# Optimization experiments

Measured on AMD Instinct MI355X. Metric: run time of the kernel, lower is better.

Reference implementation:

```python
import jax, jax.numpy as jnp
import numpy as np

N, D, E, H = 16384, 1024, 4, 4096
TEMP = 1.0

def setup_inputs() -> dict:
    key = jax.random.key(0)
    ks = jax.random.split(key, 6)
    s_in = 1.0 / np.sqrt(D)
    s_h = 1.0 / np.sqrt(H)
    s_g = 1.0 / np.sqrt(2 * D)
    return {
        "q": jax.random.normal(ks[0], (N, D), jnp.float32),
        "k": jax.random.normal(ks[1], (N, D), jnp.float32),
        "W1": jax.random.normal(ks[2], (E, D, H), jnp.float32) * s_in,
        "b1": jnp.zeros((E, H), jnp.float32),
        "W2": jax.random.normal(ks[3], (E, H, D), jnp.float32) * s_h,
        "b2": jnp.zeros((E, D), jnp.float32),
        "Wg": jax.random.normal(ks[4], (2 * D, 4), jnp.float32) * s_g,
        "bg": jnp.zeros((4,), jnp.float32),
    }

def reference(q, k, W1, b1, W2, b2, Wg, bg):
    # Run all E experts on the same tokens via batched GEMMs.
    h = jax.nn.relu(jnp.einsum('nd,edh->neh', q, W1) + b1)        # [N,E,H]
    q_pred = jnp.einsum('neh,ehd->ned', h, W2) + b2               # [N,E,D]
    # Gate: Linear(dim*2 -> 4) on concat(q,k), softmax over experts.
    logits = (jnp.concatenate([q, k], axis=-1) @ Wg + bg) / TEMP  # [N,4]
    gate = jax.nn.softmax(logits, axis=-1)                        # [N,E]
    return jnp.einsum('ned,ne->nd', q_pred, gate)                 # [N,D]
```

## Files before the change

kernel.cpp:

```cpp
#include <hip/hip_runtime.h>
#include <hip/hip_bf16.h>

#define N_TOK 16384
#define DIM   1024
#define NEXP  4
#define HID   4096

typedef __attribute__((ext_vector_type(8))) short short8;
typedef __attribute__((ext_vector_type(4))) short short4v;
typedef __attribute__((ext_vector_type(4))) float float4v;

static __device__ __forceinline__ short f2bf(float f) {
  __hip_bfloat16 h = __float2bfloat16(f);
  return *reinterpret_cast<short*>(&h);
}

#define GLOAD_LDS16(gsrc, ldst)                                                            \
  __builtin_amdgcn_global_load_lds((const __attribute__((address_space(1))) void*)(gsrc),  \
                                   (__attribute__((address_space(3))) void*)(ldst), 16, 0, 0)

__global__ void gate_kernel(const float* __restrict__ q, const float* __restrict__ k,
                            const float* __restrict__ Wg, const float* __restrict__ bg,
                            float* __restrict__ gate) {
  const int wave = threadIdx.x >> 6, lane = threadIdx.x & 63;
  const int n = blockIdx.x * 4 + wave;
  const float* qr = q + (size_t)n * DIM;
  const float* kr = k + (size_t)n * DIM;
  float s0 = 0.f, s1 = 0.f, s2 = 0.f, s3 = 0.f;
  for (int i = 0; i < DIM / 64; ++i) {
    int d = i * 64 + lane;
    float x = qr[d];
    float4 w = *(const float4*)(Wg + (size_t)d * 4);
    s0 += x * w.x; s1 += x * w.y; s2 += x * w.z; s3 += x * w.w;
    float y = kr[d];
    float4 w2 = *(const float4*)(Wg + (size_t)(DIM + d) * 4);
    s0 += y * w2.x; s1 += y * w2.y; s2 += y * w2.z; s3 += y * w2.w;
  }
  for (int off = 32; off; off >>= 1) {
    s0 += __shfl_xor(s0, off);
    s1 += __shfl_xor(s1, off);
    s2 += __shfl_xor(s2, off);
    s3 += __shfl_xor(s3, off);
  }
  if (lane == 0) {
    float l0 = s0 + bg[0], l1 = s1 + bg[1], l2 = s2 + bg[2], l3 = s3 + bg[3];
    float m = fmaxf(fmaxf(l0, l1), fmaxf(l2, l3));
    float e0 = expf(l0 - m), e1 = expf(l1 - m), e2 = expf(l2 - m), e3 = expf(l3 - m);
    float inv = 1.f / (e0 + e1 + e2 + e3);
    float4 g; g.x = e0 * inv; g.y = e1 * inv; g.z = e2 * inv; g.w = e3 * inv;
    *(float4*)(gate + (size_t)n * 4) = g;
  }
}

__global__ void convert_bf16_kernel(const float* __restrict__ in, short* __restrict__ out, int n4) {
  int stride = gridDim.x * blockDim.x;
  for (int i = blockIdx.x * blockDim.x + threadIdx.x; i < n4; i += stride) {
    float4 v = *(const float4*)(in + (size_t)i * 4);
    short4v o;
    o[0] = f2bf(v.x); o[1] = f2bf(v.y); o[2] = f2bf(v.z); o[3] = f2bf(v.w);
    *(short4v*)(out + (size_t)i * 4) = o;
  }
}

__global__ void transpose_bf16_kernel(const float* __restrict__ in, short* __restrict__ out,
                                      int R, int C) {
  __shared__ float tile[64][65];
  const size_t eoff = (size_t)blockIdx.z * (size_t)R * C;
  const float* src = in + eoff;
  short* dst = out + eoff;
  const int r0 = blockIdx.y * 64, c0 = blockIdx.x * 64;
  const int tc = threadIdx.x & 63, tr = threadIdx.x >> 6;
#pragma unroll
  for (int p = 0; p < 16; ++p) {
    int r = p * 4 + tr;
    tile[r][tc] = src[(size_t)(r0 + r) * C + (c0 + tc)];
  }
  __syncthreads();
#pragma unroll
  for (int p = 0; p < 16; ++p) {
    int i = p * 4 + tr;
    dst[(size_t)(c0 + i) * R + (r0 + tc)] = f2bf(tile[tc][i]);
  }
}

template <int MODE>
__global__ __launch_bounds__(256, 2)
void gemm_kernel(const short* __restrict__ A, const short* __restrict__ Bt, int K,
                 const float* __restrict__ bias, const float* __restrict__ gate4,
                 short* __restrict__ HsOut, float* __restrict__ FOut, int ldc, int accumulate) {
  __shared__ short sA[128 * 64];
  __shared__ short sB[128 * 64];
  const int t = threadIdx.x;
  const int m0 = blockIdx.y * 128;
  const int n0 = blockIdx.x * 128;
  const int lane = t & 63;
  const int wave = t >> 6;
  const int wm = (wave >> 1) * 64;
  const int wn = (wave & 1) * 64;
  const int r16 = lane & 15;
  const int kg = lane >> 4;

  float4v acc[4][4];
#pragma unroll
  for (int m = 0; m < 4; ++m)
#pragma unroll
    for (int n = 0; n < 4; ++n) acc[m][n] = (float4v)0.0f;

  for (int k0 = 0; k0 < K; k0 += 64) {
#pragma unroll
    for (int i = 0; i < 4; ++i) {
      int c = i * 256 + t;
      int row = c >> 3;
      int jc = (c & 7) ^ (row & 7);
      GLOAD_LDS16(A + (size_t)(m0 + row) * K + k0 + jc * 8, &sA[c * 8]);
      GLOAD_LDS16(Bt + (size_t)(n0 + row) * K + k0 + jc * 8, &sB[c * 8]);
    }
    __syncthreads();
#pragma unroll
    for (int kk = 0; kk < 2; ++kk) {
      short8 af[4], bfr[4];
#pragma unroll
      for (int m = 0; m < 4; ++m) {
        int row = wm + m * 16 + r16;
        int jc = (kk * 4 + kg) ^ (row & 7);
        af[m] = *(const short8*)&sA[row * 64 + jc * 8];
      }
#pragma unroll
      for (int n = 0; n < 4; ++n) {
        int row = wn + n * 16 + r16;
        int jc = (kk * 4 + kg) ^ (row & 7);
        bfr[n] = *(const short8*)&sB[row * 64 + jc * 8];
      }
#pragma unroll
      for (int m = 0; m < 4; ++m)
#pragma unroll
        for (int n = 0; n < 4; ++n)
          acc[m][n] = __builtin_amdgcn_mfma_f32_16x16x32_bf16(af[m], bfr[n], acc[m][n], 0, 0, 0);
    }
    __syncthreads();
  }

#pragma unroll
  for (int m = 0; m < 4; ++m) {
    int rbase = m0 + wm + m * 16 + kg * 4;
#pragma unroll
    for (int n = 0; n < 4; ++n) {
      int col = n0 + wn + n * 16 + r16;
      float bcol = bias[col];
#pragma unroll
      for (int r = 0; r < 4; ++r) {
        int grow = rbase + r;
        float g = gate4[(size_t)grow * 4];
        float v = acc[m][n][r];
        if (MODE == 1) {
          v += bcol;
          v = fmaxf(v, 0.f);
          v *= g;
          HsOut[(size_t)grow * ldc + col] = f2bf(v);
        } else {
          v += g * bcol;
          size_t oi = (size_t)grow * ldc + col;
          if (accumulate) v += FOut[oi];
          FOut[oi] = v;
        }
      }
    }
  }
}

extern "C" void kernel_launch(void* const* d_in, const int* in_sizes, int n_in,
                              void* d_out, int out_size, void* d_ws, size_t ws_size,
                              hipStream_t stream) {
  const float* q  = (const float*)d_in[0];
  const float* k  = (const float*)d_in[1];
  const float* W1 = (const float*)d_in[2];
  const float* b1 = (const float*)d_in[3];
  const float* W2 = (const float*)d_in[4];
  const float* b2 = (const float*)d_in[5];
  const float* Wg = (const float*)d_in[6];
  const float* bg = (const float*)d_in[7];
  float* out = (float*)d_out;

  char* ws = (char*)d_ws;
  size_t off = 0;
  float* gate = (float*)(ws + off); off += (size_t)N_TOK * 4 * sizeof(float);
  short* qb   = (short*)(ws + off); off += (size_t)N_TOK * DIM * 2;
  short* W1t  = (short*)(ws + off); off += (size_t)NEXP * (size_t)DIM * HID * 2;
  short* W2t  = (short*)(ws + off); off += (size_t)NEXP * (size_t)HID * DIM * 2;
  short* Hs   = (short*)(ws + off);

  size_t avail = (ws_size > off) ? (ws_size - off) : 0;
  long long mc = (long long)(avail / ((size_t)HID * 2));
  mc &= ~127LL;
  if (mc < 128) mc = 128;
  if (mc > N_TOK) mc = N_TOK;
  const int max_chunk = (int)mc;

  gate_kernel<<<dim3(N_TOK / 4), dim3(256), 0, stream>>>(q, k, Wg, bg, gate);
  convert_bf16_kernel<<<dim3(2048), dim3(256), 0, stream>>>(q, qb, N_TOK * DIM / 4);
  transpose_bf16_kernel<<<dim3(HID / 64, DIM / 64, NEXP), dim3(256), 0, stream>>>(W1, W1t, DIM, HID);
  transpose_bf16_kernel<<<dim3(DIM / 64, HID / 64, NEXP), dim3(256), 0, stream>>>(W2, W2t, HID, DIM);

  for (int cb = 0; cb < N_TOK; cb += max_chunk) {
    int rows = (N_TOK - cb < max_chunk) ? (N_TOK - cb) : max_chunk;
    for (int e = 0; e < NEXP; ++e) {
      gemm_kernel<1><<<dim3(HID / 128, rows / 128), dim3(256), 0, stream>>>(
          qb + (size_t)cb * DIM, W1t + (size_t)e * HID * DIM, DIM,
          b1 + (size_t)e * HID, gate + (size_t)cb * 4 + e,
          Hs, (float*)nullptr, HID, 0);
      gemm_kernel<2><<<dim3(DIM / 128, rows / 128), dim3(256), 0, stream>>>(
          Hs, W2t + (size_t)e * DIM * HID, HID,
          b2 + (size_t)e * DIM, gate + (size_t)cb * 4 + e,
          (short*)nullptr, out + (size_t)cb * DIM, DIM, e > 0);
    }
  }
}
```

Before: 1.372 ms.

## Use 256x256 double-buffered GEMM and fuse experts into two concatenated GEMMs

```diff
diff --git a/kernel.cpp b/kernel.cpp
--- a/kernel.cpp
+++ b/kernel.cpp
@@ -63,11 +63,10 @@
 }
 
 __global__ void transpose_bf16_kernel(const float* __restrict__ in, short* __restrict__ out,
-                                      int R, int C) {
+                                      int R, int C, int ldo, int z_row, int z_col) {
   __shared__ float tile[64][65];
-  const size_t eoff = (size_t)blockIdx.z * (size_t)R * C;
-  const float* src = in + eoff;
-  short* dst = out + eoff;
+  const int z = blockIdx.z;
+  const float* src = in + (size_t)z * R * C;
   const int r0 = blockIdx.y * 64, c0 = blockIdx.x * 64;
   const int tc = threadIdx.x & 63, tr = threadIdx.x >> 6;
 #pragma unroll
@@ -79,89 +78,167 @@
 #pragma unroll
   for (int p = 0; p < 16; ++p) {
     int i = p * 4 + tr;
-    dst[(size_t)(c0 + i) * R + (r0 + tc)] = f2bf(tile[tc][i]);
-  }
+    out[(size_t)(z * z_row + c0 + i) * ldo + z * z_col + (r0 + tc)] = f2bf(tile[tc][i]);
+  }
+}
+
+template <int QM, bool READB, bool VMWAIT>
+__device__ __forceinline__ void do_phase(const short* pA, const short* pB,
+                                         short8 (&af)[4], short8 (&bf)[4],
+                                         float4v (&acc)[8][4]) {
+#pragma unroll
+  for (int m4 = 0; m4 < 4; ++m4)
+    af[m4] = *(const short8*)(pA + QM * 4096 + m4 * 1024);
+  if (READB) {
+#pragma unroll
+    for (int n4 = 0; n4 < 4; ++n4)
+      bf[n4] = *(const short8*)(pB + n4 * 1024);
+  }
+  __builtin_amdgcn_s_barrier();
+  asm volatile("s_waitcnt lgkmcnt(0)" ::: "memory");
+  __builtin_amdgcn_sched_barrier(0);
+  __builtin_amdgcn_s_setprio(1);
+#pragma unroll
+  for (int m4 = 0; m4 < 4; ++m4)
+#pragma unroll
+    for (int n4 = 0; n4 < 4; ++n4)
+      acc[QM * 4 + m4][n4] =
+          __builtin_amdgcn_mfma_f32_16x16x32_bf16(af[m4], bf[n4], acc[QM * 4 + m4][n4], 0, 0, 0);
+  __builtin_amdgcn_s_setprio(0);
+  if (VMWAIT) asm volatile("s_waitcnt vmcnt(0)" ::: "memory");
+  __builtin_amdgcn_sched_barrier(0);
+  __builtin_amdgcn_s_barrier();
 }
 
 template <int MODE>
-__global__ __launch_bounds__(256, 2)
-void gemm_kernel(const short* __restrict__ A, const short* __restrict__ Bt, int K,
-                 const float* __restrict__ bias, const float* __restrict__ gate4,
-                 short* __restrict__ HsOut, float* __restrict__ FOut, int ldc, int accumulate) {
-  __shared__ short sA[128 * 64];
-  __shared__ short sB[128 * 64];
-  const int t = threadIdx.x;
-  const int m0 = blockIdx.y * 128;
-  const int n0 = blockIdx.x * 128;
-  const int lane = t & 63;
-  const int wave = t >> 6;
-  const int wm = (wave >> 1) * 64;
-  const int wn = (wave & 1) * 64;
-  const int r16 = lane & 15;
-  const int kg = lane >> 4;
-
-  float4v acc[4][4];
-#pragma unroll
-  for (int m = 0; m < 4; ++m)
+__global__ __launch_bounds__(512, 2)
+void gemm256(const short* __restrict__ A, const short* __restrict__ Bt, int K, int ldb,
+             int NTN, const float* __restrict__ bias, const float* __restrict__ gate,
+             int ecol_off, int e0, int e1, int accum,
+             short* __restrict__ OutB, float* __restrict__ OutF, int ldc) {
+  __shared__ short sA[32768];
+  __shared__ short sB[32768];
+
+  const int nwg = gridDim.x;
+  const int NTM = nwg / NTN;
+  {
+  }
+  int bid = blockIdx.x;
+  int qd = nwg >> 3, rm = nwg & 7;
+  int xcd = bid & 7, idx = bid >> 3;
+  int swz = (xcd < rm ? xcd * (qd + 1) : rm * (qd + 1) + (xcd - rm) * qd) + idx;
+  const int tpg = 8 * NTN;
+  int g = swz / tpg;
+  int lg = swz % tpg;
+  int gm0 = g * 8;
+  int gsz = NTM - gm0; if (gsz > 8) gsz = 8;
+  const int tile_m = gm0 + lg % gsz;
+  const int tile_n = lg / gsz;
+  const int m0 = tile_m * 256;
+  const int n0 = tile_n * 256;
+
+  const int tid = threadIdx.x;
+  const int lane = tid & 63;
+  const int wid = tid >> 6;
+  const int wm = wid >> 2, wn = wid & 3;
+  const int r16 = lane & 15, kg = lane >> 4;
+  const int rowL = tid >> 3;
+  const int gc8 = (((tid & 7) ^ (rowL & 7)) * 8);
+  const int st8 = tid * 8;
+  const int sw0 = (kg ^ (r16 & 7)) * 8;
+  const int sw1 = ((4 + kg) ^ (r16 & 7)) * 8;
+  const int aoff0 = (wm * 128 + r16) * 64 + sw0;
+  const int aoff1 = (wm * 128 + r16) * 64 + sw1;
+  const int boff0 = (wn * 64 + r16) * 64 + sw0;
+  const int boff1 = (wn * 64 + r16) * 64 + sw1;
+
+  const short* aSrc = A + (size_t)(m0 + rowL) * K + gc8;
+  const short* bSrc = Bt + (size_t)(n0 + rowL) * ldb + gc8;
+
+  float4v acc[8][4];
+#pragma unroll
+  for (int m = 0; m < 8; ++m)
 #pragma unroll
     for (int n = 0; n < 4; ++n) acc[m][n] = (float4v)0.0f;
 
-  for (int k0 = 0; k0 < K; k0 += 64) {
-#pragma unroll
-    for (int i = 0; i < 4; ++i) {
-      int c = i * 256 + t;
-      int row = c >> 3;
-      int jc = (c & 7) ^ (row & 7);
-      GLOAD_LDS16(A + (size_t)(m0 + row) * K + k0 + jc * 8, &sA[c * 8]);
-      GLOAD_LDS16(Bt + (size_t)(n0 + row) * K + k0 + jc * 8, &sB[c * 8]);
-    }
-    __syncthreads();
-#pragma unroll
-    for (int kk = 0; kk < 2; ++kk) {
-      short8 af[4], bfr[4];
-#pragma unroll
-      for (int m = 0; m < 4; ++m) {
-        int row = wm + m * 16 + r16;
-        int jc = (kk * 4 + kg) ^ (row & 7);
-        af[m] = *(const short8*)&sA[row * 64 + jc * 8];
+#pragma unroll
+  for (int s = 0; s < 4; ++s) {
+    GLOAD_LDS16(aSrc + (size_t)s * 64 * K, sA + s * 4096 + st8);
+    GLOAD_LDS16(bSrc + (size_t)s * 64 * ldb, sB + s * 4096 + st8);
+  }
+  asm volatile("s_waitcnt vmcnt(0)" ::: "memory");
+  __builtin_amdgcn_s_barrier();
+
+  const int T = K >> 6;
+  const short* aN = aSrc + 64;
+  const short* bN = bSrc + 64;
+  int cur = 0;
+  short8 af[4], bf[4];
+  for (int t = 0; t < T; ++t) {
+    const int co = cur << 14;
+    const int po = (cur ^ 1) << 14;
+    const bool next = (t + 1 < T);
+    const short* pA0 = sA + co + aoff0;
+    const short* pA1 = sA + co + aoff1;
+    const short* pB0 = sB + co + boff0;
+    const short* pB1 = sB + co + boff1;
+    if (next) {
+#pragma unroll
+      for (int s = 0; s < 4; ++s) GLOAD_LDS16(aN + (size_t)s * 64 * K, sA + po + s * 4096 + st8);
+    }
+    do_phase<0, true, false>(pA0, pB0, af, bf, acc);
+    if (next) {
+#pragma unroll
+      for (int s = 0; s < 4; ++s) GLOAD_LDS16(bN + (size_t)s * 64 * ldb, sB + po + s * 4096 + st8);
+    }
+    do_phase<1, false, false>(pA0, pB0, af, bf, acc);
+    do_phase<0, true, false>(pA1, pB1, af, bf, acc);
+    do_phase<1, false, true>(pA1, pB1, af, bf, acc);
+    aN += 64;
+    bN += 64;
+    cur ^= 1;
+  }
+
+  const int rowb = m0 + wm * 128 + kg * 4;
+  const int colb = n0 + wn * 64 + r16;
+  if (MODE == 1) {
+    const int e = (ecol_off + n0) >> 12;
+#pragma unroll
+    for (int m4 = 0; m4 < 8; ++m4) {
+      int r0a = rowb + m4 * 16;
+#pragma unroll
+      for (int r = 0; r < 4; ++r) {
+        int row = r0a + r;
+        float g = gate[(size_t)row * 4 + e];
+#pragma unroll
+        for (int n4 = 0; n4 < 4; ++n4) {
+          int col = colb + n4 * 16;
+          float v = acc[m4][n4][r] + bias[ecol_off + col];
+          OutB[(size_t)row * ldc + col] = f2bf(fmaxf(v, 0.f) * g);
+        }
       }
-#pragma unroll
-      for (int n = 0; n < 4; ++n) {
-        int row = wn + n * 16 + r16;
-        int jc = (kk * 4 + kg) ^ (row & 7);
-        bfr[n] = *(const short8*)&sB[row * 64 + jc * 8];
-      }
-#pragma unroll
-      for (int m = 0; m < 4; ++m)
-#pragma unroll
-        for (int n = 0; n < 4; ++n)
-          acc[m][n] = __builtin_amdgcn_mfma_f32_16x16x32_bf16(af[m], bfr[n], acc[m][n], 0, 0, 0);
-    }
-    __syncthreads();
-  }
-
-#pragma unroll
-  for (int m = 0; m < 4; ++m) {
-    int rbase = m0 + wm + m * 16 + kg * 4;
-#pragma unroll
-    for (int n = 0; n < 4; ++n) {
-      int col = n0 + wn + n * 16 + r16;
-      float bcol = bias[col];
+    }
+  } else {
+#pragma unroll
+    for (int m4 = 0; m4 < 8; ++m4) {
+      int r0a = rowb + m4 * 16;
 #pragma unroll
       for (int r = 0; r < 4; ++r) {
-        int grow = rbase + r;
-        float g = gate4[(size_t)grow * 4];
-        float v = acc[m][n][r];
-        if (MODE == 1) {
-          v += bcol;
-          v = fmaxf(v, 0.f);
-          v *= g;
-          HsOut[(size_t)grow * ldc + col] = f2bf(v);
-        } else {
-          v += g * bcol;
-          size_t oi = (size_t)grow * ldc + col;
-          if (accumulate) v += FOut[oi];
-          FOut[oi] = v;
+        int row = r0a + r;
+        float4 gv = *(const float4*)(gate + (size_t)row * 4);
+#pragma unroll
+        for (int n4 = 0; n4 < 4; ++n4) {
+          int col = colb + n4 * 16;
+          float bt;
+          if (e0 == 0 && e1 == 4)
+            bt = gv.x * bias[col] + gv.y * bias[1024 + col] + gv.z * bias[2048 + col] +
+                 gv.w * bias[3072 + col];
+          else
+            bt = gate[(size_t)row * 4 + e0] * bias[e0 * 1024 + col];
+          float v = acc[m4][n4][r] + bt;
+          size_t oi = (size_t)row * ldc + col;
+          if (accum) v += OutF[oi];
+          OutF[oi] = v;
         }
       }
     }
@@ -186,32 +263,43 @@
   float* gate = (float*)(ws + off); off += (size_t)N_TOK * 4 * sizeof(float);
   short* qb   = (short*)(ws + off); off += (size_t)N_TOK * DIM * 2;
   short* W1t  = (short*)(ws + off); off += (size_t)NEXP * (size_t)DIM * HID * 2;
-  short* W2t  = (short*)(ws + off); off += (size_t)NEXP * (size_t)HID * DIM * 2;
-  short* Hs   = (short*)(ws + off);
-
-  size_t avail = (ws_size > off) ? (ws_size - off) : 0;
-  long long mc = (long long)(avail / ((size_t)HID * 2));
-  mc &= ~127LL;
-  if (mc < 128) mc = 128;
-  if (mc > N_TOK) mc = N_TOK;
-  const int max_chunk = (int)mc;
+  short* W2t2 = (short*)(ws + off); off += (size_t)NEXP * (size_t)HID * DIM * 2;
+  const size_t fixed = off;
 
   gate_kernel<<<dim3(N_TOK / 4), dim3(256), 0, stream>>>(q, k, Wg, bg, gate);
   convert_bf16_kernel<<<dim3(2048), dim3(256), 0, stream>>>(q, qb, N_TOK * DIM / 4);
-  transpose_bf16_kernel<<<dim3(HID / 64, DIM / 64, NEXP), dim3(256), 0, stream>>>(W1, W1t, DIM, HID);
-  transpose_bf16_kernel<<<dim3(DIM / 64, HID / 64, NEXP), dim3(256), 0, stream>>>(W2, W2t, HID, DIM);
-
-  for (int cb = 0; cb < N_TOK; cb += max_chunk) {
-    int rows = (N_TOK - cb < max_chunk) ? (N_TOK - cb) : max_chunk;
-    for (int e = 0; e < NEXP; ++e) {
-      gemm_kernel<1><<<dim3(HID / 128, rows / 128), dim3(256), 0, stream>>>(
-          qb + (size_t)cb * DIM, W1t + (size_t)e * HID * DIM, DIM,
-          b1 + (size_t)e * HID, gate + (size_t)cb * 4 + e,
-          Hs, (float*)nullptr, HID, 0);
-      gemm_kernel<2><<<dim3(DIM / 128, rows / 128), dim3(256), 0, stream>>>(
-          Hs, W2t + (size_t)e * DIM * HID, HID,
-          b2 + (size_t)e * DIM, gate + (size_t)cb * 4 + e,
-          (short*)nullptr, out + (size_t)cb * DIM, DIM, e > 0);
-    }
-  }
-}
+  transpose_bf16_kernel<<<dim3(HID / 64, DIM / 64, NEXP), dim3(256), 0, stream>>>(
+      W1, W1t, DIM, HID, DIM, HID, 0);
+  transpose_bf16_kernel<<<dim3(DIM / 64, HID / 64, NEXP), dim3(256), 0, stream>>>(
+      W2, W2t2, HID, DIM, NEXP * HID, 0, HID);
+
+  size_t avail = (ws_size > fixed) ? ws_size - fixed : 0;
+  const size_t hs_concat = (size_t)N_TOK * (NEXP * HID) * 2;
+
+  if (avail >= hs_concat) {
+    short* Hs = (short*)(ws + fixed);
+    gemm256<1><<<dim3((N_TOK / 256) * (NEXP * HID / 256)), dim3(512), 0, stream>>>(
+        qb, W1t, DIM, DIM, NEXP * HID / 256, b1, gate, 0, 0, 0, 0, Hs, nullptr, NEXP * HID);
+    gemm256<2><<<dim3((N_TOK / 256) * (DIM / 256)), dim3(512), 0, stream>>>(
+        Hs, W2t2, NEXP * HID, NEXP * HID, DIM / 256, b2, gate, 0, 0, 4, 0, nullptr, out, DIM);
+  } else {
+    short* Hs = (short*)(ws + fixed);
+    long long mc = (long long)(avail / ((size_t)HID * 2));
+    mc &= ~255LL;
+    if (mc < 256) mc = 256;
+    if (mc > N_TOK) mc = N_TOK;
+    for (int cb = 0; cb < N_TOK; cb += (int)mc) {
+      int rows = (N_TOK - cb < (int)mc) ? (N_TOK - cb) : (int)mc;
+      int NTM = rows / 256;
+      for (int e = 0; e < NEXP; ++e) {
+        gemm256<1><<<dim3(NTM * (HID / 256)), dim3(512), 0, stream>>>(
+            qb + (size_t)cb * DIM, W1t + (size_t)e * HID * DIM, DIM, DIM, HID / 256,
+            b1, gate + (size_t)cb * 4, e * HID, 0, 0, 0, Hs, nullptr, HID);
+        gemm256<2><<<dim3(NTM * (DIM / 256)), dim3(512), 0, stream>>>(
+            Hs, W2t2 + (size_t)e * HID, HID, NEXP * HID, DIM / 256,
+            b2, gate + (size_t)cb * 4, 0, e, e + 1, (e > 0) ? 1 : 0, nullptr,
+            out + (size_t)cb * DIM, DIM);
+      }
+    }
+  }
+}
```

Measured after the change: 1.664 ms. +21.3%, slower.
